# Kernel tuning notes

Hardware: AMD Instinct MI355X
Metric: run time of the kernel (lower is better)

## Reference

```python
import jax, jax.numpy as jnp
import numpy as np

GAMMA = 1.0


def setup_inputs() -> dict:
    key = jax.random.key(0)
    kx, ky = jax.random.split(key)
    x = jax.random.normal(kx, (8192, 256), dtype=jnp.float32)
    y = jax.random.normal(ky, (8192, 256), dtype=jnp.float32)
    return {"x": x, "y": y}


def reference(x, y):
    # (same math as the broadcast subtract-square-sum, without the O(n*m*d) temp)
    x = x.reshape(-1, x.shape[-1])
    y = y.reshape(-1, y.shape[-1])
    x_sq = jnp.sum(x * x, axis=-1)  # (n,)
    y_sq = jnp.sum(y * y, axis=-1)  # (m,)
    cross = jnp.einsum('nd,md->nm', x, y)  # (n, m)
    dist_sq = x_sq[:, None] + y_sq[None, :] - 2.0 * cross
    dist_sq = jnp.maximum(dist_sq, 0.0)  # clamp tiny negatives from fp error
    return jnp.exp(-GAMMA * dist_sq)
```

## Files before the change

### kernel.cpp

```cpp
#include <hip/hip_runtime.h>

#define NROWS 8192
#define DDIM  256
#define BM    128
#define BN    128
#define BK    64

typedef __attribute__((ext_vector_type(8))) short bf16x8;
typedef __attribute__((ext_vector_type(4))) float f32x4;

static __device__ __forceinline__ unsigned short f2bf(float f) {
    unsigned u = __float_as_uint(f);
    u += 0x7fff + ((u >> 16) & 1);
    return (unsigned short)(u >> 16);
}

__global__ __launch_bounds__(256) void rbf_prep_kernel(
    const float* __restrict__ x, const float* __restrict__ y,
    unsigned short* __restrict__ xb, unsigned short* __restrict__ yb,
    float* __restrict__ xsq, float* __restrict__ ysq)
{
    const int lane = threadIdx.x & 63;
    const int wid  = threadIdx.x >> 6;
    int row = blockIdx.x * 4 + wid;
    const float* src; unsigned short* dst; float* sq; int r;
    if (row < NROWS) { src = x; dst = xb; sq = xsq; r = row; }
    else             { src = y; dst = yb; sq = ysq; r = row - NROWS; }

    const float4 v = ((const float4*)(src + (size_t)r * DDIM))[lane];
    ushort4 b;
    b.x = f2bf(v.x); b.y = f2bf(v.y); b.z = f2bf(v.z); b.w = f2bf(v.w);
    ((ushort4*)(dst + (size_t)r * DDIM))[lane] = b;

    float s = v.x * v.x + v.y * v.y + v.z * v.z + v.w * v.w;
    #pragma unroll
    for (int o = 32; o > 0; o >>= 1) s += __shfl_down(s, o);
    if (lane == 0) sq[r] = s;
}

__global__ __launch_bounds__(256) void rbf_gemm_kernel(
    const unsigned short* __restrict__ A,
    const unsigned short* __restrict__ B,
    const float* __restrict__ xsq, const float* __restrict__ ysq,
    float* __restrict__ out)
{
    __shared__ unsigned short As[BM * BK];
    __shared__ unsigned short Bs[BN * BK];

    const int t    = threadIdx.x;
    const int lane = t & 63;
    const int wid  = t >> 6;
    const int wr   = wid >> 1;
    const int wc   = wid & 1;
    const int brow = blockIdx.y * BM;
    const int bcol = blockIdx.x * BN;

    f32x4 acc[4][4] = {};

    const int rr = lane & 15;
    const int kq = lane >> 4;

    for (int kt = 0; kt < DDIM; kt += BK) {
        #pragma unroll
        for (int i = 0; i < 4; ++i) {
            const int idx = (i * 256 + t) * 8;
            const int r   = idx >> 6;
            const int c   = idx & 63;
            __builtin_amdgcn_global_load_lds(
                (const __attribute__((address_space(1))) unsigned int*)(A + (size_t)(brow + r) * DDIM + kt + c),
                (__attribute__((address_space(3))) unsigned int*)(As + idx), 16, 0, 0);
            __builtin_amdgcn_global_load_lds(
                (const __attribute__((address_space(1))) unsigned int*)(B + (size_t)(bcol + r) * DDIM + kt + c),
                (__attribute__((address_space(3))) unsigned int*)(Bs + idx), 16, 0, 0);
        }
        __syncthreads();

        #pragma unroll
        for (int ks = 0; ks < 2; ++ks) {
            bf16x8 a[4], b[4];
            const int ko = ks * 32 + kq * 8;
            #pragma unroll
            for (int m = 0; m < 4; ++m)
                a[m] = *(const bf16x8*)(As + (wr * 64 + m * 16 + rr) * BK + ko);
            #pragma unroll
            for (int n = 0; n < 4; ++n)
                b[n] = *(const bf16x8*)(Bs + (wc * 64 + n * 16 + rr) * BK + ko);
            #pragma unroll
            for (int m = 0; m < 4; ++m)
                #pragma unroll
                for (int n = 0; n < 4; ++n)
                    acc[m][n] = __builtin_amdgcn_mfma_f32_16x16x32_bf16(b[n], a[m], acc[m][n], 0, 0, 0);
        }
        __syncthreads();
    }

    const int cl = lane & 15;
    const int rq = lane >> 4;
    #pragma unroll
    for (int m = 0; m < 4; ++m) {
        const int row = brow + wr * 64 + m * 16 + cl;
        const float xsv = xsq[row];
        float* orow = out + (size_t)row * NROWS;
        #pragma unroll
        for (int n = 0; n < 4; ++n) {
            const int col = bcol + wc * 64 + n * 16 + rq * 4;
            const float4 ysv = *(const float4*)(ysq + col);
            float4 o;
            o.x = __expf(-fmaxf(xsv + ysv.x - 2.0f * acc[m][n][0], 0.0f));
            o.y = __expf(-fmaxf(xsv + ysv.y - 2.0f * acc[m][n][1], 0.0f));
            o.z = __expf(-fmaxf(xsv + ysv.z - 2.0f * acc[m][n][2], 0.0f));
            o.w = __expf(-fmaxf(xsv + ysv.w - 2.0f * acc[m][n][3], 0.0f));
            *(float4*)(orow + col) = o;
        }
    }
}

extern "C" void kernel_launch(void* const* d_in, const int* in_sizes, int n_in,
                              void* d_out, int out_size, void* d_ws, size_t ws_size,
                              hipStream_t stream) {
    const float* x = (const float*)d_in[0];
    const float* y = (const float*)d_in[1];
    float* out = (float*)d_out;

    unsigned short* xb = (unsigned short*)d_ws;
    unsigned short* yb = xb + (size_t)NROWS * DDIM;
    float* xsq = (float*)(yb + (size_t)NROWS * DDIM);
    float* ysq = xsq + NROWS;

    rbf_prep_kernel<<<dim3((2 * NROWS) / 4), 256, 0, stream>>>(x, y, xb, yb, xsq, ysq);
    rbf_gemm_kernel<<<dim3(NROWS / BN, NROWS / BM), 256, 0, stream>>>(xb, yb, xsq, ysq, out);
}
```

Measured before the change: 310.3 us.

## Double-buffer LDS tiles to overlap global loads with MFMA compute

Splits the A/B shared-memory tiles into two buffers and fully unrolls the four K-steps. The global-to-LDS load for the next K tile is issued before the MFMA work on the current tile, and each step needs one barrier instead of two. The aim is to hide load latency behind compute. In exchange, LDS use per block doubles to 64 KB, which can reduce how many blocks fit on a CU.

```diff
diff --git a/kernel.cpp b/kernel.cpp
--- a/kernel.cpp
+++ b/kernel.cpp
@@ -44,8 +44,8 @@
     const float* __restrict__ xsq, const float* __restrict__ ysq,
     float* __restrict__ out)
 {
-    __shared__ unsigned short As[BM * BK];
-    __shared__ unsigned short Bs[BN * BK];
+    __shared__ unsigned short As[2][BM * BK];
+    __shared__ unsigned short Bs[2][BN * BK];
 
     const int t    = threadIdx.x;
     const int lane = t & 63;
@@ -60,39 +60,54 @@
     const int rr = lane & 15;
     const int kq = lane >> 4;
 
-    for (int kt = 0; kt < DDIM; kt += BK) {
-        #pragma unroll
-        for (int i = 0; i < 4; ++i) {
-            const int idx = (i * 256 + t) * 8;
-            const int r   = idx >> 6;
-            const int c   = idx & 63;
-            __builtin_amdgcn_global_load_lds(
-                (const __attribute__((address_space(1))) unsigned int*)(A + (size_t)(brow + r) * DDIM + kt + c),
-                (__attribute__((address_space(3))) unsigned int*)(As + idx), 16, 0, 0);
-            __builtin_amdgcn_global_load_lds(
-                (const __attribute__((address_space(1))) unsigned int*)(B + (size_t)(bcol + r) * DDIM + kt + c),
-                (__attribute__((address_space(3))) unsigned int*)(Bs + idx), 16, 0, 0);
+    #define STAGE(buf, kt)                                                              \
+        _Pragma("unroll")                                                               \
+        for (int i = 0; i < 4; ++i) {                                                   \
+            const int idx = (i * 256 + t) * 8;                                          \
+            const int r   = idx >> 6;                                                   \
+            const int c   = idx & 63;                                                   \
+            __builtin_amdgcn_global_load_lds(                                           \
+                (const __attribute__((address_space(1))) unsigned int*)(A + (size_t)(brow + r) * DDIM + (kt) + c), \
+                (__attribute__((address_space(3))) unsigned int*)(&As[buf][idx]), 16, 0, 0); \
+            __builtin_amdgcn_global_load_lds(                                           \
+                (const __attribute__((address_space(1))) unsigned int*)(B + (size_t)(bcol + r) * DDIM + (kt) + c), \
+                (__attribute__((address_space(3))) unsigned int*)(&Bs[buf][idx]), 16, 0, 0); \
         }
-        __syncthreads();
 
-        #pragma unroll
-        for (int ks = 0; ks < 2; ++ks) {
-            bf16x8 a[4], b[4];
-            const int ko = ks * 32 + kq * 8;
-            #pragma unroll
-            for (int m = 0; m < 4; ++m)
-                a[m] = *(const bf16x8*)(As + (wr * 64 + m * 16 + rr) * BK + ko);
-            #pragma unroll
-            for (int n = 0; n < 4; ++n)
-                b[n] = *(const bf16x8*)(Bs + (wc * 64 + n * 16 + rr) * BK + ko);
-            #pragma unroll
-            for (int m = 0; m < 4; ++m)
-                #pragma unroll
-                for (int n = 0; n < 4; ++n)
-                    acc[m][n] = __builtin_amdgcn_mfma_f32_16x16x32_bf16(b[n], a[m], acc[m][n], 0, 0, 0);
+    #define COMPUTE(buf)                                                                \
+        _Pragma("unroll")                                                               \
+        for (int ks = 0; ks < 2; ++ks) {                                                \
+            bf16x8 a[4], b[4];                                                          \
+            const int ko = ks * 32 + kq * 8;                                            \
+            _Pragma("unroll")                                                           \
+            for (int m = 0; m < 4; ++m)                                                 \
+                a[m] = *(const bf16x8*)(&As[buf][(wr * 64 + m * 16 + rr) * BK + ko]);   \
+            _Pragma("unroll")                                                           \
+            for (int n = 0; n < 4; ++n)                                                 \
+                b[n] = *(const bf16x8*)(&Bs[buf][(wc * 64 + n * 16 + rr) * BK + ko]);   \
+            _Pragma("unroll")                                                           \
+            for (int m = 0; m < 4; ++m)                                                 \
+                _Pragma("unroll")                                                       \
+                for (int n = 0; n < 4; ++n)                                             \
+                    acc[m][n] = __builtin_amdgcn_mfma_f32_16x16x32_bf16(b[n], a[m], acc[m][n], 0, 0, 0); \
         }
-        __syncthreads();
-    }
+
+    STAGE(0, 0)
+    __syncthreads();
+
+    STAGE(1, 64)
+    COMPUTE(0)
+    __syncthreads();
+
+    STAGE(0, 128)
+    COMPUTE(1)
+    __syncthreads();
+
+    STAGE(1, 192)
+    COMPUTE(0)
+    __syncthreads();
+
+    COMPUTE(1)
 
     const int cl = lane & 15;
     const int rq = lane >> 4;
```

After: 317.1 us. +2.2%, slower.
